# Kernel tuning notes

Hardware: AMD Instinct MI355X
Metric: run time of the kernel (lower is better)

Reference implementation:

```python
import jax, jax.numpy as jnp
import numpy as np
import math

DIM = 2048
N_HEADS = 16
HEAD_DIM = DIM // N_HEADS
B, S = 2, 2048
EPS = 1e-6


def rms_norm(x, w):
    return x * jax.lax.rsqrt(jnp.mean(x * x, axis=-1, keepdims=True) + EPS) * w


def rotate(x, cos, sin):
    x1, x2 = jnp.split(x, 2, axis=-1)
    rotated = jnp.concatenate((-x2, x1), axis=-1)
    return x * cos + rotated * sin


def setup_inputs() -> dict:
    key = jax.random.key(0)
    ks = jax.random.split(key, 16)
    half = HEAD_DIM // 2
    inv_freq = 1.0 / (10000.0 ** (jnp.arange(0, half, dtype=jnp.float32) / half))
    t = jnp.arange(S, dtype=jnp.float32)
    freqs = jnp.einsum('s,d->sd', t, inv_freq)
    emb = jnp.concatenate((freqs, freqs), axis=-1)  # [S, HEAD_DIM]
    cos = jnp.cos(emb)[None, None]  # [1,1,S,HEAD_DIM]
    sin = jnp.sin(emb)[None, None]
    # causal additive mask [1,1,S,S]
    causal = jnp.triu(jnp.full((S, S), -1e9, dtype=jnp.float32), k=1)[None, None]
    sc = 0.02
    return {
        'x': jax.random.normal(ks[0], (B, S, DIM), jnp.float32),
        'cos': cos,
        'sin': sin,
        'mask': causal,
        'attn_norm_w': jnp.ones((DIM,), jnp.float32),
        'ffn_norm_w': jnp.ones((DIM,), jnp.float32),
        'wq': jax.random.normal(ks[1], (DIM, DIM), jnp.float32) * sc,
        'wk': jax.random.normal(ks[2], (DIM, DIM), jnp.float32) * sc,
        'wv': jax.random.normal(ks[3], (DIM, DIM), jnp.float32) * sc,
        'wo': jax.random.normal(ks[4], (DIM, DIM), jnp.float32) * sc,
        'w1': jax.random.normal(ks[5], (DIM, 4 * DIM), jnp.float32) * sc,
        'w2': jax.random.normal(ks[6], (4 * DIM, DIM), jnp.float32) * sc,
        'w3': jax.random.normal(ks[7], (DIM, 4 * DIM), jnp.float32) * sc,
    }


def reference(x, cos, sin, mask, attn_norm_w, ffn_norm_w, wq, wk, wv, wo, w1, w2, w3):
    b, s, d = x.shape
    h = rms_norm(x, attn_norm_w)
    q = (h @ wq).reshape(b, s, N_HEADS, HEAD_DIM).transpose(0, 2, 1, 3)
    k = (h @ wk).reshape(b, s, N_HEADS, HEAD_DIM).transpose(0, 2, 1, 3)
    v = (h @ wv).reshape(b, s, N_HEADS, HEAD_DIM).transpose(0, 2, 1, 3)
    q = rotate(q, cos, sin)
    k = rotate(k, cos, sin)
    attn = jnp.einsum('bhqd,bhkd->bhqk', q, k) / math.sqrt(HEAD_DIM)
    attn = attn + mask
    attn = jax.nn.softmax(attn, axis=-1)
    out = jnp.einsum('bhqk,bhkd->bhqd', attn, v)
    out = out.transpose(0, 2, 1, 3).reshape(b, s, d)
    x = x + out @ wo
    h = rms_norm(x, ffn_norm_w)
    x = x + (jax.nn.silu(h @ w1) * (h @ w3)) @ w2
    return x
```

## Files before the change

### kernel.cpp

```cpp
#include <hip/hip_runtime.h>

#define DIM 2048
#define HDIM 128
#define NH 16
#define SEQ 2048
#define BATCH 2
#define MROWS (BATCH*SEQ)
#define QKP 6144

typedef __attribute__((ext_vector_type(8))) short short8;
typedef __attribute__((ext_vector_type(4))) float f32x4;

__device__ __forceinline__ unsigned short f2bf(float f) {
  union { float f; unsigned u; } v; v.f = f;
  unsigned r = v.u + 0x7FFFu + ((v.u >> 16) & 1u);
  return (unsigned short)(r >> 16);
}
__device__ __forceinline__ float bf2f(unsigned short b) {
  union { unsigned u; float f; } v; v.u = ((unsigned)b) << 16;
  return v.f;
}

__device__ __forceinline__ void gload16(const void* g, void* l) {
  __builtin_amdgcn_global_load_lds((const __attribute__((address_space(1))) unsigned int*)g,
                                   (__attribute__((address_space(3))) unsigned int*)l,
                                   16, 0, 0);
}

__global__ __launch_bounds__(256) void rmsnorm_kernel(const float* __restrict__ x,
                                                      const float* __restrict__ w,
                                                      unsigned short* __restrict__ out) {
  const int row = blockIdx.x;
  const int t = threadIdx.x;
  const float* xr = x + (size_t)row * DIM;
  float4 v0 = ((const float4*)xr)[t*2];
  float4 v1 = ((const float4*)xr)[t*2+1];
  float ss = v0.x*v0.x + v0.y*v0.y + v0.z*v0.z + v0.w*v0.w
           + v1.x*v1.x + v1.y*v1.y + v1.z*v1.z + v1.w*v1.w;
  #pragma unroll
  for (int i = 1; i < 64; i <<= 1) ss += __shfl_xor(ss, i);
  __shared__ float red[4];
  if ((t & 63) == 0) red[t >> 6] = ss;
  __syncthreads();
  float sum = red[0] + red[1] + red[2] + red[3];
  float sc = rsqrtf(sum * (1.0f/DIM) + 1e-6f);
  const float* wr = w + t*8;
  unsigned short ob[8];
  ob[0] = f2bf(v0.x*sc*wr[0]); ob[1] = f2bf(v0.y*sc*wr[1]);
  ob[2] = f2bf(v0.z*sc*wr[2]); ob[3] = f2bf(v0.w*sc*wr[3]);
  ob[4] = f2bf(v1.x*sc*wr[4]); ob[5] = f2bf(v1.y*sc*wr[5]);
  ob[6] = f2bf(v1.z*sc*wr[6]); ob[7] = f2bf(v1.w*sc*wr[7]);
  uint4 pk;
  pk.x = (unsigned)ob[0] | ((unsigned)ob[1] << 16);
  pk.y = (unsigned)ob[2] | ((unsigned)ob[3] << 16);
  pk.z = (unsigned)ob[4] | ((unsigned)ob[5] << 16);
  pk.w = (unsigned)ob[6] | ((unsigned)ob[7] << 16);
  *((uint4*)(out + (size_t)row*DIM + t*8)) = pk;
}

__global__ __launch_bounds__(256) void transpose_w_kernel(const float* __restrict__ W,
                                                          unsigned short* __restrict__ Wt,
                                                          int K, int N) {
  __shared__ float tile[32][33];
  const int k0 = blockIdx.x*32, n0 = blockIdx.y*32;
  const int tx = threadIdx.x, ty = threadIdx.y;
  #pragma unroll
  for (int i=0;i<4;i++) tile[ty+i*8][tx] = W[(size_t)(k0+ty+i*8)*N + n0+tx];
  __syncthreads();
  #pragma unroll
  for (int i=0;i<4;i++) Wt[(size_t)(n0+ty+i*8)*K + k0+tx] = f2bf(tile[tx][ty+i*8]);
}

__global__ __launch_bounds__(256) void transpose_v_kernel(const unsigned short* __restrict__ v,
                                                          int vpitch,
                                                          unsigned short* __restrict__ vt) {
  __shared__ unsigned short tile[32][33];
  const int b = blockIdx.z;
  const int s0 = blockIdx.x*32, c0 = blockIdx.y*32;
  const int tx = threadIdx.x, ty = threadIdx.y;
  #pragma unroll
  for (int i=0;i<4;i++) tile[ty+i*8][tx] = v[((size_t)(b*SEQ + s0+ty+i*8))*vpitch + c0+tx];
  __syncthreads();
  #pragma unroll
  for (int i=0;i<4;i++) vt[((size_t)(b*DIM + c0+ty+i*8))*SEQ + s0+tx] = tile[tx][ty+i*8];
}

__global__ __launch_bounds__(256) void rope_qk(unsigned short* __restrict__ qk,
                                               const float* __restrict__ cosb,
                                               const float* __restrict__ sinb) {
  const size_t idx = (size_t)blockIdx.x * 256 + threadIdx.x;
  const int d = (int)(idx & 63);
  const int h = (int)((idx >> 6) & 31);
  const int row = (int)(idx >> 11);
  const int s = row & (SEQ-1);
  const size_t base = (size_t)row * QKP + h*HDIM + d;
  float a  = bf2f(qk[base]);
  float bq = bf2f(qk[base+64]);
  float c1 = cosb[s*HDIM + d],    s1 = sinb[s*HDIM + d];
  float c2 = cosb[s*HDIM + d+64], s2 = sinb[s*HDIM + d+64];
  qk[base]    = f2bf(a*c1 - bq*s1);
  qk[base+64] = f2bf(bq*c2 + a*s2);
}

template<int BM, int EPI>
__global__ __launch_bounds__(512, 2) void gemm_pipe(const unsigned short* __restrict__ A,
                                                    const unsigned short* __restrict__ Bt,
                                                    const float* __restrict__ aux,
                                                    void* __restrict__ outp,
                                                    int M, int N, int K) {
  constexpr int MF = BM / 32;
  constexpr int ASLOT = BM * 32;
  constexpr int SLOT = (BM + 256) * 32;
  extern __shared__ unsigned short ldsd[];
  const int tid = threadIdx.x, l = tid & 63, wid = tid >> 6;
  const int wm = wid >> 2, wn = wid & 3;
  const int lr = l & 15, lg = l >> 4;

  const int nbx = N >> 8;
  const int nwg = gridDim.x;
  const int sb = ((int)blockIdx.x & 7) * (nwg >> 3) + ((int)blockIdx.x >> 3);
  const int bx = sb % nbx, by = sb / nbx;
  const int m0 = by * BM, n0 = bx * 256;

  const int swz  = (((l & 3) ^ ((l >> 3) & 3)) << 3);
  const int rsub = l >> 2;

  const int kx = ((lg ^ ((lr >> 1) & 3)) << 3);
  int aoff[MF];
  #pragma unroll
  for (int mf = 0; mf < MF; mf++) aoff[mf] = (wm*(BM/2) + mf*16 + lr) * 32 + kx;
  int boff[4];
  #pragma unroll
  for (int nf = 0; nf < 4; nf++) boff[nf] = ASLOT + (wn*64 + nf*16 + lr) * 32 + kx;

  f32x4 acc[MF][4] = {};
  const int nt = K >> 5;

  auto STAGE = [&](int tt) {
    unsigned short* sA = ldsd + (tt & 3) * SLOT;
    unsigned short* sB = sA + ASLOT;
    const int k0 = tt << 5;
    #pragma unroll
    for (int c = 0; c < 2; c++) {
      const int rb = (c*8 + wid) * 16;
      gload16(Bt + (size_t)(n0 + rb + rsub) * K + k0 + swz, sB + rb*32);
    }
    if constexpr (BM == 256) {
      #pragma unroll
      for (int c = 0; c < 2; c++) {
        const int rb = (c*8 + wid) * 16;
        gload16(A + (size_t)(m0 + rb + rsub) * K + k0 + swz, sA + rb*32);
      }
    } else {
      const int rb = wid * 16;
      gload16(A + (size_t)(m0 + rb + rsub) * K + k0 + swz, sA + rb*32);
    }
  };

  STAGE(0); STAGE(1); STAGE(2);

  for (int tt = 0; tt < nt; ++tt) {
    if (tt + 3 < nt) {
      STAGE(tt + 3);
      if constexpr (BM == 256) asm volatile("s_waitcnt vmcnt(12)" ::: "memory");
      else                     asm volatile("s_waitcnt vmcnt(9)" ::: "memory");
    } else {
      asm volatile("s_waitcnt vmcnt(0)" ::: "memory");
    }
    __builtin_amdgcn_s_barrier();
    const unsigned short* slot = ldsd + (tt & 3) * SLOT;
    short8 af[MF], bfv[4];
    #pragma unroll
    for (int mf = 0; mf < MF; mf++) af[mf] = *(const short8*)&slot[aoff[mf]];
    #pragma unroll
    for (int nf = 0; nf < 4; nf++) bfv[nf] = *(const short8*)&slot[boff[nf]];
    __builtin_amdgcn_s_setprio(1);
    #pragma unroll
    for (int mf = 0; mf < MF; mf++)
      #pragma unroll
      for (int nf = 0; nf < 4; nf++)
        acc[mf][nf] = __builtin_amdgcn_mfma_f32_16x16x32_bf16(af[mf], bfv[nf], acc[mf][nf], 0, 0, 0);
    __builtin_amdgcn_s_setprio(0);
    __builtin_amdgcn_s_barrier();
  }

  #pragma unroll
  for (int mf = 0; mf < MF; mf++)
    #pragma unroll
    for (int nf = 0; nf < 4; nf++)
      #pragma unroll
      for (int r = 0; r < 4; r++) {
        const int row = m0 + wm*(BM/2) + mf*16 + lg*4 + r;
        const int col = n0 + wn*64 + nf*16 + lr;
        const size_t idx = (size_t)row * N + col;
        if constexpr (EPI == 0) {
          ((unsigned short*)outp)[idx] = f2bf(acc[mf][nf][r]);
        } else if constexpr (EPI == 1) {
          ((float*)outp)[idx] = acc[mf][nf][r] + aux[idx];
        } else {
          float g = acc[mf][nf][r];
          float u = bf2f(((unsigned short*)outp)[idx]);
          float sg = u / (1.0f + __expf(-u));
          ((unsigned short*)outp)[idx] = f2bf(sg * g);
        }
      }
}

__global__ __launch_bounds__(256, 2) void attn_kernel(const unsigned short* __restrict__ q,
                                                      const unsigned short* __restrict__ k,
                                                      const unsigned short* __restrict__ vt,
                                                      unsigned short* __restrict__ ao) {
  const int t = threadIdx.x, lane = t & 63, w = t >> 6;
  const int qt = (int)gridDim.x - 1 - (int)blockIdx.x;
  const int bh = blockIdx.y;
  const int b = bh >> 4, h = bh & 15;
  const int lr = lane & 15, lg = lane >> 4;
  const int q0w = qt*128 + w*32;

  __shared__ __attribute__((aligned(16))) unsigned short Kb[64*128];
  __shared__ __attribute__((aligned(16))) unsigned short Vb[128*64];
  __shared__ __attribute__((aligned(16))) unsigned short Ones[16*72];
  __shared__ __attribute__((aligned(16))) unsigned short P[4][32*72];
  unsigned short* pw = &P[w][0];

  for (int idx = t; idx < 16*72; idx += 256) Ones[idx] = (idx < 72) ? 0x3F80 : 0;

  short8 aq[2][4];
  {
    const unsigned short* qp = q + ((size_t)(b*SEQ + q0w + lr))*QKP + h*HDIM;
    #pragma unroll
    for (int mf=0;mf<2;mf++)
      #pragma unroll
      for (int c=0;c<4;c++) aq[mf][c] = *(const short8*)(qp + (size_t)mf*16*QKP + c*32 + lg*8);
  }

  f32x4 accO[2][8] = {};
  f32x4 accO9[2] = {};
  float mrow[2][4];
  #pragma unroll
  for (int mf=0;mf<2;mf++)
    #pragma unroll
    for (int r=0;r<4;r++) mrow[mf][r] = -3.0e38f;

  const float scale = 0.08838834764831845f;
  const unsigned short* kg = k + (size_t)(b*SEQ)*QKP + h*HDIM;
  const unsigned short* vg = vt + (size_t)(bh*HDIM)*SEQ;

  const unsigned short* kga[4]; const unsigned short* vga[4];
  unsigned short* kld[4]; unsigned short* vld[4];
  #pragma unroll
  for (int i=0;i<4;i++) {
    const int D = i*256 + t;
    const int rk = D >> 4, jk = D & 15;
    kga[i] = kg + (size_t)rk*QKP + ((jk ^ (rk & 7)) * 8);
    const int rv = D >> 3, jv = D & 7;
    vga[i] = vg + (size_t)rv*SEQ + ((jv ^ (rv & 7)) * 8);
    kld[i] = &Kb[i*2048 + w*512];
    vld[i] = &Vb[i*2048 + w*512];
  }

  const int KV_END = qt*128 + 128;

  for (int kv0 = 0; kv0 < KV_END; kv0 += 64) {
    #pragma unroll
    for (int i=0;i<4;i++) gload16(kga[i] + (size_t)kv0*QKP, kld[i]);
    #pragma unroll
    for (int i=0;i<4;i++) gload16(vga[i] + kv0, vld[i]);
    __syncthreads();

    if (kv0 < q0w + 32) {
      f32x4 sc[2][4] = {};
      #pragma unroll
      for (int blk=0;blk<4;blk++) {
        const int krow = blk*16 + lr;
        const int sw = (krow & 7) << 3;
        #pragma unroll
        for (int c=0;c<4;c++) {
          short8 bk = *(const short8*)&Kb[krow*128 + ((c*32 + lg*8) ^ sw)];
          sc[0][blk] = __builtin_amdgcn_mfma_f32_16x16x32_bf16(aq[0][c], bk, sc[0][blk], 0,0,0);
          sc[1][blk] = __builtin_amdgcn_mfma_f32_16x16x32_bf16(aq[1][c], bk, sc[1][blk], 0,0,0);
        }
      }
      #pragma unroll
      for (int mf=0;mf<2;mf++)
        #pragma unroll
        for (int blk=0;blk<4;blk++)
          #pragma unroll
          for (int r=0;r<4;r++) sc[mf][blk][r] *= scale;
      if (kv0 + 63 > q0w) {
        #pragma unroll
        for (int mf=0;mf<2;mf++)
          #pragma unroll
          for (int blk=0;blk<4;blk++)
            #pragma unroll
            for (int r=0;r<4;r++)
              if (kv0 + blk*16 + lr > q0w + mf*16 + lg*4 + r) sc[mf][blk][r] = -1.0e30f;
      }
      float pm[2][4];
      #pragma unroll
      for (int mf=0;mf<2;mf++)
        #pragma unroll
        for (int r=0;r<4;r++) {
          float m0 = fmaxf(fmaxf(sc[mf][0][r], sc[mf][1][r]), fmaxf(sc[mf][2][r], sc[mf][3][r]));
          #pragma unroll
          for (int x=1;x<16;x<<=1) m0 = fmaxf(m0, __shfl_xor(m0, x));
          pm[mf][r] = m0;
        }
      int need = 0;
      #pragma unroll
      for (int mf=0;mf<2;mf++)
        #pragma unroll
        for (int r=0;r<4;r++) need |= (pm[mf][r] > mrow[mf][r] + 8.0f) ? 1 : 0;
      if (__any(need)) {
        #pragma unroll
        for (int mf=0;mf<2;mf++)
          #pragma unroll
          for (int r=0;r<4;r++) {
            const float mn = fmaxf(mrow[mf][r], pm[mf][r]);
            const float fc = __expf(mrow[mf][r] - mn);
            mrow[mf][r] = mn;
            #pragma unroll
            for (int n=0;n<8;n++) accO[mf][n][r] *= fc;
            accO9[mf][r] *= fc;
          }
      }
      #pragma unroll
      for (int mf=0;mf<2;mf++)
        #pragma unroll
        for (int blk=0;blk<4;blk++)
          #pragma unroll
          for (int r=0;r<4;r++) {
            const float p = __expf(sc[mf][blk][r] - mrow[mf][r]);
            pw[(mf*16 + lg*4 + r)*72 + blk*16 + lr] = f2bf(p);
          }
      short8 ap[2][2];
      #pragma unroll
      for (int mf=0;mf<2;mf++)
        #pragma unroll
        for (int ks=0;ks<2;ks++) ap[mf][ks] = *(const short8*)&pw[(mf*16 + lr)*72 + ks*32 + lg*8];
      #pragma unroll
      for (int n=0;n<8;n++) {
        #pragma unroll
        for (int ks=0;ks<2;ks++) {
          const int vrow = n*16 + lr;
          const int sw = (vrow & 7) << 3;
          short8 bv = *(const short8*)&Vb[vrow*64 + ((ks*32 + lg*8) ^ sw)];
          accO[0][n] = __builtin_amdgcn_mfma_f32_16x16x32_bf16(ap[0][ks], bv, accO[0][n], 0,0,0);
          accO[1][n] = __builtin_amdgcn_mfma_f32_16x16x32_bf16(ap[1][ks], bv, accO[1][n], 0,0,0);
        }
      }
      #pragma unroll
      for (int ks=0;ks<2;ks++) {
        short8 bv9 = *(const short8*)&Ones[lr*72 + ks*32 + lg*8];
        accO9[0] = __builtin_amdgcn_mfma_f32_16x16x32_bf16(ap[0][ks], bv9, accO9[0], 0,0,0);
        accO9[1] = __builtin_amdgcn_mfma_f32_16x16x32_bf16(ap[1][ks], bv9, accO9[1], 0,0,0);
      }
    }
    __syncthreads();
  }

  #pragma unroll
  for (int mf=0;mf<2;mf++)
    #pragma unroll
    for (int r=0;r<4;r++) {
      const float lv = __shfl(accO9[mf][r], lane & 48);
      const float inv = 1.0f / lv;
      const size_t row = (size_t)(b*SEQ + q0w + mf*16 + lg*4 + r);
      #pragma unroll
      for (int n=0;n<8;n++)
        ao[row*DIM + h*HDIM + n*16 + lr] = f2bf(accO[mf][n][r] * inv);
    }
}

extern "C" void kernel_launch(void* const* d_in, const int* in_sizes, int n_in,
                              void* d_out, int out_size, void* d_ws, size_t ws_size,
                              hipStream_t stream) {
  (void)in_sizes; (void)n_in; (void)out_size; (void)ws_size;
  const float* x    = (const float*)d_in[0];
  const float* cosb = (const float*)d_in[1];
  const float* sinb = (const float*)d_in[2];
  const float* anw  = (const float*)d_in[4];
  const float* fnw  = (const float*)d_in[5];
  const float* wq   = (const float*)d_in[6];
  const float* wk   = (const float*)d_in[7];
  const float* wv   = (const float*)d_in[8];
  const float* wo   = (const float*)d_in[9];
  const float* w1   = (const float*)d_in[10];
  const float* w2   = (const float*)d_in[11];
  const float* w3   = (const float*)d_in[12];

  char* ws = (char*)d_ws;
  const size_t MB = 1048576;
  unsigned short* h     = (unsigned short*)(ws);
  unsigned short* qkvb  = (unsigned short*)(ws + 16*MB);
  unsigned short* mid   = qkvb;
  unsigned short* aob   = (unsigned short*)(ws + 67*MB);
  char* wt              = ws + 84*MB;
  unsigned short* wqkvT = (unsigned short*)wt;
  unsigned short* vtb   = (unsigned short*)wt;
  unsigned short* woT   = (unsigned short*)wt;
  unsigned short* wfT   = (unsigned short*)wt;
  float* x1f = (float*)d_out;

  dim3 b256(256);
  dim3 tb(32, 8);
  constexpr unsigned LDS256 = (256+256)*32*2*4;
  constexpr unsigned LDS128 = (128+256)*32*2*4;

  rmsnorm_kernel<<<dim3(MROWS), b256, 0, stream>>>(x, anw, h);

  transpose_w_kernel<<<dim3(64,64), tb, 0, stream>>>(wq, wqkvT,           2048, 2048);
  transpose_w_kernel<<<dim3(64,64), tb, 0, stream>>>(wk, wqkvT + 4194304, 2048, 2048);
  transpose_w_kernel<<<dim3(64,64), tb, 0, stream>>>(wv, wqkvT + 8388608, 2048, 2048);

  gemm_pipe<256,0><<<dim3(384), dim3(512), LDS256, stream>>>(h, wqkvT, nullptr, qkvb, MROWS, 6144, 2048);

  rope_qk<<<dim3(32768), b256, 0, stream>>>(qkvb, cosb, sinb);

  transpose_v_kernel<<<dim3(64,64,2), tb, 0, stream>>>(qkvb + 4096, QKP, vtb);

  attn_kernel<<<dim3(16,32), b256, 0, stream>>>(qkvb, qkvb + 2048, vtb, aob);

  transpose_w_kernel<<<dim3(64,64), tb, 0, stream>>>(wo, woT, 2048, 2048);
  gemm_pipe<128,1><<<dim3(256), dim3(512), LDS128, stream>>>(aob, woT, x, x1f, MROWS, 2048, 2048);

  rmsnorm_kernel<<<dim3(MROWS), b256, 0, stream>>>(x1f, fnw, h);

  transpose_w_kernel<<<dim3(64,256), tb, 0, stream>>>(w1, wfT, 2048, 8192);
  gemm_pipe<256,0><<<dim3(512), dim3(512), LDS256, stream>>>(h, wfT, nullptr, mid, MROWS, 8192, 2048);
  transpose_w_kernel<<<dim3(64,256), tb, 0, stream>>>(w3, wfT, 2048, 8192);
  gemm_pipe<256,3><<<dim3(512), dim3(512), LDS256, stream>>>(h, wfT, nullptr, mid, MROWS, 8192, 2048);

  transpose_w_kernel<<<dim3(256,64), tb, 0, stream>>>(w2, wfT, 8192, 2048);
  gemm_pipe<128,1><<<dim3(256), dim3(512), LDS128, stream>>>(mid, wfT, x1f, (float*)d_out, MROWS, 2048, 8192);
}
```

Before: 902.3 us.

## Restructure GEMM mainloop into 64-wide K tiles with phased half-tile prefetch

Rewrites the bf16 GEMM main loop so each step covers 64-wide K tiles in a double buffer, with A and B each split into halves. Loads are spread across eight compute phases so each half-tile is prefetched while MFMAs run on the other buffer. B fragments are held in registers across four phases. LDS layout moves to a row-XOR swizzle over 8-element chunks, keeping the same LDS footprint. The goal is fewer barriers per K step and better overlap of global-to-LDS traffic with matrix math, at the cost of more registers and a more intricate barrier and vmcnt schedule.

After: 856.5 us. 1.05x faster.

```diff
diff --git a/kernel.cpp b/kernel.cpp
--- a/kernel.cpp
+++ b/kernel.cpp
@@ -10,6 +10,8 @@
 
 typedef __attribute__((ext_vector_type(8))) short short8;
 typedef __attribute__((ext_vector_type(4))) float f32x4;
+
+template<int N> struct ic { static constexpr int value = N; };
 
 __device__ __forceinline__ unsigned short f2bf(float f) {
   union { float f; unsigned u; } v; v.f = f;
@@ -108,13 +110,17 @@
                                                     const float* __restrict__ aux,
                                                     void* __restrict__ outp,
                                                     int M, int N, int K) {
-  constexpr int MF = BM / 32;
-  constexpr int ASLOT = BM * 32;
-  constexpr int SLOT = (BM + 256) * 32;
+  constexpr int HRA = BM/2;
+  constexpr int MF  = BM/32;
+  constexpr int APP = MF/4;
+  constexpr int LA  = BM/128;
+  constexpr int AHS = HRA*64;
+  constexpr int BB  = 4*AHS;
   extern __shared__ unsigned short ldsd[];
   const int tid = threadIdx.x, l = tid & 63, wid = tid >> 6;
   const int wm = wid >> 2, wn = wid & 3;
   const int lr = l & 15, lg = l >> 4;
+  const int bh = wn >> 1, brow0 = (wn & 1)*64;
 
   const int nbx = N >> 8;
   const int nwg = gridDim.x;
@@ -122,66 +128,90 @@
   const int bx = sb % nbx, by = sb / nbx;
   const int m0 = by * BM, n0 = bx * 256;
 
-  const int swz  = (((l & 3) ^ ((l >> 3) & 3)) << 3);
-  const int rsub = l >> 2;
-
-  const int kx = ((lg ^ ((lr >> 1) & 3)) << 3);
-  int aoff[MF];
-  #pragma unroll
-  for (int mf = 0; mf < MF; mf++) aoff[mf] = (wm*(BM/2) + mf*16 + lr) * 32 + kx;
-  int boff[4];
-  #pragma unroll
-  for (int nf = 0; nf < 4; nf++) boff[nf] = ASLOT + (wn*64 + nf*16 + lr) * 32 + kx;
-
-  f32x4 acc[MF][4] = {};
-  const int nt = K >> 5;
-
-  auto STAGE = [&](int tt) {
-    unsigned short* sA = ldsd + (tt & 3) * SLOT;
-    unsigned short* sB = sA + ASLOT;
-    const int k0 = tt << 5;
-    #pragma unroll
-    for (int c = 0; c < 2; c++) {
-      const int rb = (c*8 + wid) * 16;
-      gload16(Bt + (size_t)(n0 + rb + rsub) * K + k0 + swz, sB + rb*32);
-    }
-    if constexpr (BM == 256) {
-      #pragma unroll
-      for (int c = 0; c < 2; c++) {
-        const int rb = (c*8 + wid) * 16;
-        gload16(A + (size_t)(m0 + rb + rsub) * K + k0 + swz, sA + rb*32);
-      }
-    } else {
-      const int rb = wid * 16;
-      gload16(A + (size_t)(m0 + rb + rsub) * K + k0 + swz, sA + rb*32);
+  auto stageA = [&](int db, int half, int tile) {
+    #pragma unroll
+    for (int c=0;c<LA;c++) {
+      const int D = c*512 + tid;
+      const int row = D>>3, j = D&7;
+      gload16(A + (size_t)(m0 + half*HRA + row)*K + (tile<<6) + ((j ^ (row&7))<<3),
+              &ldsd[(db*2+half)*AHS + D*8]);
     }
   };
-
-  STAGE(0); STAGE(1); STAGE(2);
-
-  for (int tt = 0; tt < nt; ++tt) {
-    if (tt + 3 < nt) {
-      STAGE(tt + 3);
-      if constexpr (BM == 256) asm volatile("s_waitcnt vmcnt(12)" ::: "memory");
-      else                     asm volatile("s_waitcnt vmcnt(9)" ::: "memory");
-    } else {
-      asm volatile("s_waitcnt vmcnt(0)" ::: "memory");
+  auto stageB = [&](int db, int half, int tile) {
+    #pragma unroll
+    for (int c=0;c<2;c++) {
+      const int D = c*512 + tid;
+      const int row = D>>3, j = D&7;
+      gload16(Bt + (size_t)(n0 + half*128 + row)*K + (tile<<6) + ((j ^ (row&7))<<3),
+              &ldsd[BB + (db*2+half)*8192 + D*8]);
     }
-    __builtin_amdgcn_s_barrier();
-    const unsigned short* slot = ldsd + (tt & 3) * SLOT;
-    short8 af[MF], bfv[4];
-    #pragma unroll
-    for (int mf = 0; mf < MF; mf++) af[mf] = *(const short8*)&slot[aoff[mf]];
-    #pragma unroll
-    for (int nf = 0; nf < 4; nf++) bfv[nf] = *(const short8*)&slot[boff[nf]];
-    __builtin_amdgcn_s_setprio(1);
-    #pragma unroll
-    for (int mf = 0; mf < MF; mf++)
-      #pragma unroll
-      for (int nf = 0; nf < 4; nf++)
-        acc[mf][nf] = __builtin_amdgcn_mfma_f32_16x16x32_bf16(af[mf], bfv[nf], acc[mf][nf], 0, 0, 0);
-    __builtin_amdgcn_s_setprio(0);
-    __builtin_amdgcn_s_barrier();
+  };
+
+  f32x4 acc[MF][4] = {};
+  short8 bfrag[4][2];
+  const int ntile = K >> 6;
+
+  stageB(0,0,0); stageB(0,1,0);
+  stageA(0,0,0); stageA(0,1,0);
+  stageB(1,0,1); stageB(1,1,1);
+  asm volatile("s_waitcnt vmcnt(4)" ::: "memory");
+  __builtin_amdgcn_s_barrier();
+
+  for (int T = 0; T < ntile; T += 2) {
+    const bool notlast = (T + 2 < ntile);
+    auto phase = [&](auto PC) {
+      constexpr int P = decltype(PC)::value;
+      constexpr int hi = P >> 2;
+      constexpr int p  = P & 3;
+      if constexpr (p == 0) {
+        #pragma unroll
+        for (int nf=0;nf<4;nf++) {
+          const int rh = brow0 + nf*16 + lr;
+          #pragma unroll
+          for (int ks=0;ks<2;ks++) {
+            const int j = (ks*4 + lg) ^ (rh & 7);
+            bfrag[nf][ks] = *(const short8*)&ldsd[BB + (hi*2+bh)*8192 + rh*64 + j*8];
+          }
+        }
+      }
+      short8 afr[APP][2];
+      #pragma unroll
+      for (int mi=0;mi<APP;mi++) {
+        const int rh = (p*APP+mi)*16 + lr;
+        #pragma unroll
+        for (int ks=0;ks<2;ks++) {
+          const int j = (ks*4 + lg) ^ (rh & 7);
+          afr[mi][ks] = *(const short8*)&ldsd[(hi*2+wm)*AHS + rh*64 + j*8];
+        }
+      }
+      if constexpr (P == 0)      stageA(1, 0, T+1);
+      else if constexpr (P == 1) stageA(1, 1, T+1);
+      else if constexpr (P == 2) { if (notlast) stageB(0, 0, T+2); }
+      else if constexpr (P == 3) { if (notlast) stageB(0, 1, T+2); }
+      else if constexpr (P == 4) { if (notlast) stageA(0, 0, T+2); }
+      else if constexpr (P == 5) { if (notlast) stageA(0, 1, T+2); }
+      else if constexpr (P == 6) { if (notlast) stageB(1, 0, T+3); }
+      else if constexpr (P == 7) { if (notlast) stageB(1, 1, T+3); }
+      if constexpr (P == 3 || P == 7) {
+        if (notlast) { asm volatile("s_waitcnt vmcnt(4)" ::: "memory"); }
+        else         { asm volatile("s_waitcnt vmcnt(0)" ::: "memory"); }
+      }
+      __builtin_amdgcn_sched_barrier(0);
+      __builtin_amdgcn_s_barrier();
+      __builtin_amdgcn_sched_barrier(0);
+      __builtin_amdgcn_s_setprio(1);
+      #pragma unroll
+      for (int mi=0;mi<APP;mi++)
+        #pragma unroll
+        for (int nf=0;nf<4;nf++)
+          #pragma unroll
+          for (int ks=0;ks<2;ks++)
+            acc[p*APP+mi][nf] = __builtin_amdgcn_mfma_f32_16x16x32_bf16(afr[mi][ks], bfrag[nf][ks], acc[p*APP+mi][nf], 0,0,0);
+      __builtin_amdgcn_s_setprio(0);
+      __builtin_amdgcn_s_barrier();
+    };
+    phase(ic<0>{}); phase(ic<1>{}); phase(ic<2>{}); phase(ic<3>{});
+    phase(ic<4>{}); phase(ic<5>{}); phase(ic<6>{}); phase(ic<7>{});
   }
 
   #pragma unroll
@@ -190,7 +220,7 @@
     for (int nf = 0; nf < 4; nf++)
       #pragma unroll
       for (int r = 0; r < 4; r++) {
-        const int row = m0 + wm*(BM/2) + mf*16 + lg*4 + r;
+        const int row = m0 + wm*HRA + mf*16 + lg*4 + r;
         const int col = n0 + wn*64 + nf*16 + lr;
         const size_t idx = (size_t)row * N + col;
         if constexpr (EPI == 0) {
@@ -404,8 +434,8 @@
 
   dim3 b256(256);
   dim3 tb(32, 8);
-  constexpr unsigned LDS256 = (256+256)*32*2*4;
-  constexpr unsigned LDS128 = (128+256)*32*2*4;
+  constexpr unsigned LDS256 = 131072;
+  constexpr unsigned LDS128 = 98304;
 
   rmsnorm_kernel<<<dim3(MROWS), b256, 0, stream>>>(x, anw, h);
 
```

## Replace pipelined 256-wide GEMM with simple 128x128 single-buffer GEMM

Applied to the files above, without the earlier changes.

Swaps the 4-stage, 512-thread GEMM with large 256x256/128x256 tiles for a 256-thread kernel using 128x128 tiles, a single LDS buffer and plain __syncthreads. The tiles move to static shared memory, an XCD-aware block swizzle is added, and occupancy rises to 3 blocks per CU. Load-compute overlap within a block is dropped in exchange for more resident blocks and more tiles in the grid. Smaller tiles also mean less reuse per load.

Result: slower. 967.9 us (+7.3%).

```diff
diff --git a/kernel.cpp b/kernel.cpp
--- a/kernel.cpp
+++ b/kernel.cpp
@@ -102,96 +102,74 @@
   qk[base+64] = f2bf(bq*c2 + a*s2);
 }
 
-template<int BM, int EPI>
-__global__ __launch_bounds__(512, 2) void gemm_pipe(const unsigned short* __restrict__ A,
-                                                    const unsigned short* __restrict__ Bt,
-                                                    const float* __restrict__ aux,
-                                                    void* __restrict__ outp,
-                                                    int M, int N, int K) {
-  constexpr int MF = BM / 32;
-  constexpr int ASLOT = BM * 32;
-  constexpr int SLOT = (BM + 256) * 32;
-  extern __shared__ unsigned short ldsd[];
-  const int tid = threadIdx.x, l = tid & 63, wid = tid >> 6;
-  const int wm = wid >> 2, wn = wid & 3;
+template<int EPI>
+__global__ __launch_bounds__(256, 3) void gemm_m97(const unsigned short* __restrict__ A,
+                                                   const unsigned short* __restrict__ Bt,
+                                                   const float* __restrict__ aux,
+                                                   void* __restrict__ outp,
+                                                   int M, int N, int K) {
+  __shared__ unsigned short As[128*32];
+  __shared__ unsigned short Bs[128*32];
+  const int tid = threadIdx.x, l = tid & 63, w = tid >> 6;
+  const int wr = w >> 1, wc = w & 1;
   const int lr = l & 15, lg = l >> 4;
 
-  const int nbx = N >> 8;
-  const int nwg = gridDim.x;
-  const int sb = ((int)blockIdx.x & 7) * (nwg >> 3) + ((int)blockIdx.x >> 3);
-  const int bx = sb % nbx, by = sb / nbx;
-  const int m0 = by * BM, n0 = bx * 256;
-
-  const int swz  = (((l & 3) ^ ((l >> 3) & 3)) << 3);
-  const int rsub = l >> 2;
-
-  const int kx = ((lg ^ ((lr >> 1) & 3)) << 3);
-  int aoff[MF];
-  #pragma unroll
-  for (int mf = 0; mf < MF; mf++) aoff[mf] = (wm*(BM/2) + mf*16 + lr) * 32 + kx;
-  int boff[4];
-  #pragma unroll
-  for (int nf = 0; nf < 4; nf++) boff[nf] = ASLOT + (wn*64 + nf*16 + lr) * 32 + kx;
-
-  f32x4 acc[MF][4] = {};
-  const int nt = K >> 5;
-
-  auto STAGE = [&](int tt) {
-    unsigned short* sA = ldsd + (tt & 3) * SLOT;
-    unsigned short* sB = sA + ASLOT;
-    const int k0 = tt << 5;
-    #pragma unroll
-    for (int c = 0; c < 2; c++) {
-      const int rb = (c*8 + wid) * 16;
-      gload16(Bt + (size_t)(n0 + rb + rsub) * K + k0 + swz, sB + rb*32);
+  const int nbx = N >> 7;
+  const int SW = ((nbx & 7) == 0) ? (nbx >> 3) : 1;
+  const int xcd = (int)blockIdx.x & 7;
+  const int ii  = (int)blockIdx.x >> 3;
+  const int by = ii / SW;
+  const int bx = xcd * SW + (ii % SW);
+  const int m0 = by * 128, n0 = bx * 128;
+
+  const int srow = tid >> 2;
+  const int jsw = ((tid & 3) ^ (srow & 3)) << 3;
+  const unsigned short* srcA[2];
+  const unsigned short* srcB[2];
+  #pragma unroll
+  for (int c=0;c<2;c++) {
+    srcA[c] = A  + (size_t)(m0 + c*64 + srow)*K + jsw;
+    srcB[c] = Bt + (size_t)(n0 + c*64 + srow)*K + jsw;
+  }
+  unsigned short* dstA = As + tid*8;
+  unsigned short* dstB = Bs + tid*8;
+
+  const int jc = ((lg ^ (lr & 3)) << 3);
+  const unsigned short* ldsA = As + (wr*64 + lr)*32 + jc;
+  const unsigned short* ldsB = Bs + (wc*64 + lr)*32 + jc;
+
+  f32x4 acc[4][4] = {};
+  const int ntile = K >> 5;
+  int kO = 0;
+
+  for (int t = 0; t < ntile; ++t, kO += 32) {
+    #pragma unroll
+    for (int c=0;c<2;c++) {
+      gload16(srcA[c] + kO, dstA + c*2048);
+      gload16(srcB[c] + kO, dstB + c*2048);
     }
-    if constexpr (BM == 256) {
-      #pragma unroll
-      for (int c = 0; c < 2; c++) {
-        const int rb = (c*8 + wid) * 16;
-        gload16(A + (size_t)(m0 + rb + rsub) * K + k0 + swz, sA + rb*32);
-      }
-    } else {
-      const int rb = wid * 16;
-      gload16(A + (size_t)(m0 + rb + rsub) * K + k0 + swz, sA + rb*32);
-    }
-  };
-
-  STAGE(0); STAGE(1); STAGE(2);
-
-  for (int tt = 0; tt < nt; ++tt) {
-    if (tt + 3 < nt) {
-      STAGE(tt + 3);
-      if constexpr (BM == 256) asm volatile("s_waitcnt vmcnt(12)" ::: "memory");
-      else                     asm volatile("s_waitcnt vmcnt(9)" ::: "memory");
-    } else {
-      asm volatile("s_waitcnt vmcnt(0)" ::: "memory");
-    }
-    __builtin_amdgcn_s_barrier();
-    const unsigned short* slot = ldsd + (tt & 3) * SLOT;
-    short8 af[MF], bfv[4];
-    #pragma unroll
-    for (int mf = 0; mf < MF; mf++) af[mf] = *(const short8*)&slot[aoff[mf]];
-    #pragma unroll
-    for (int nf = 0; nf < 4; nf++) bfv[nf] = *(const short8*)&slot[boff[nf]];
-    __builtin_amdgcn_s_setprio(1);
-    #pragma unroll
-    for (int mf = 0; mf < MF; mf++)
-      #pragma unroll
-      for (int nf = 0; nf < 4; nf++)
-        acc[mf][nf] = __builtin_amdgcn_mfma_f32_16x16x32_bf16(af[mf], bfv[nf], acc[mf][nf], 0, 0, 0);
-    __builtin_amdgcn_s_setprio(0);
-    __builtin_amdgcn_s_barrier();
+    __syncthreads();
+    short8 af[4], bf[4];
+    #pragma unroll
+    for (int mf=0;mf<4;mf++) af[mf] = *(const short8*)(ldsA + mf*512);
+    #pragma unroll
+    for (int nf=0;nf<4;nf++) bf[nf] = *(const short8*)(ldsB + nf*512);
+    #pragma unroll
+    for (int mf=0;mf<4;mf++)
+      #pragma unroll
+      for (int nf=0;nf<4;nf++)
+        acc[mf][nf] = __builtin_amdgcn_mfma_f32_16x16x32_bf16(af[mf], bf[nf], acc[mf][nf], 0,0,0);
+    __syncthreads();
   }
 
   #pragma unroll
-  for (int mf = 0; mf < MF; mf++)
+  for (int mf = 0; mf < 4; mf++)
     #pragma unroll
     for (int nf = 0; nf < 4; nf++)
       #pragma unroll
       for (int r = 0; r < 4; r++) {
-        const int row = m0 + wm*(BM/2) + mf*16 + lg*4 + r;
-        const int col = n0 + wn*64 + nf*16 + lr;
+        const int row = m0 + wr*64 + mf*16 + lg*4 + r;
+        const int col = n0 + wc*64 + nf*16 + lr;
         const size_t idx = (size_t)row * N + col;
         if constexpr (EPI == 0) {
           ((unsigned short*)outp)[idx] = f2bf(acc[mf][nf][r]);
@@ -404,8 +382,6 @@
 
   dim3 b256(256);
   dim3 tb(32, 8);
-  constexpr unsigned LDS256 = (256+256)*32*2*4;
-  constexpr unsigned LDS128 = (128+256)*32*2*4;
 
   rmsnorm_kernel<<<dim3(MROWS), b256, 0, stream>>>(x, anw, h);
 
@@ -413,7 +389,7 @@
   transpose_w_kernel<<<dim3(64,64), tb, 0, stream>>>(wk, wqkvT + 4194304, 2048, 2048);
   transpose_w_kernel<<<dim3(64,64), tb, 0, stream>>>(wv, wqkvT + 8388608, 2048, 2048);
 
-  gemm_pipe<256,0><<<dim3(384), dim3(512), LDS256, stream>>>(h, wqkvT, nullptr, qkvb, MROWS, 6144, 2048);
+  gemm_m97<0><<<dim3(32*48), b256, 0, stream>>>(h, wqkvT, nullptr, qkvb, MROWS, 6144, 2048);
 
   rope_qk<<<dim3(32768), b256, 0, stream>>>(qkvb, cosb, sinb);
 
@@ -422,15 +398,15 @@
   attn_kernel<<<dim3(16,32), b256, 0, stream>>>(qkvb, qkvb + 2048, vtb, aob);
 
   transpose_w_kernel<<<dim3(64,64), tb, 0, stream>>>(wo, woT, 2048, 2048);
-  gemm_pipe<128,1><<<dim3(256), dim3(512), LDS128, stream>>>(aob, woT, x, x1f, MROWS, 2048, 2048);
+  gemm_m97<1><<<dim3(32*16), b256, 0, stream>>>(aob, woT, x, x1f, MROWS, 2048, 2048);
 
   rmsnorm_kernel<<<dim3(MROWS), b256, 0, stream>>>(x1f, fnw, h);
 
   transpose_w_kernel<<<dim3(64,256), tb, 0, stream>>>(w1, wfT, 2048, 8192);
-  gemm_pipe<256,0><<<dim3(512), dim3(512), LDS256, stream>>>(h, wfT, nullptr, mid, MROWS, 8192, 2048);
+  gemm_m97<0><<<dim3(32*64), b256, 0, stream>>>(h, wfT, nullptr, mid, MROWS, 8192, 2048);
   transpose_w_kernel<<<dim3(64,256), tb, 0, stream>>>(w3, wfT, 2048, 8192);
-  gemm_pipe<256,3><<<dim3(512), dim3(512), LDS256, stream>>>(h, wfT, nullptr, mid, MROWS, 8192, 2048);
+  gemm_m97<3><<<dim3(32*64), b256, 0, stream>>>(h, wfT, nullptr, mid, MROWS, 8192, 2048);
 
   transpose_w_kernel<<<dim3(256,64), tb, 0, stream>>>(w2, wfT, 8192, 2048);
-  gemm_pipe<128,1><<<dim3(256), dim3(512), LDS128, stream>>>(mid, wfT, x1f, (float*)d_out, MROWS, 2048, 8192);
-}
+  gemm_m97<1><<<dim3(32*16), b256, 0, stream>>>(mid, wfT, x1f, (float*)d_out, MROWS, 2048, 8192);
+}
```
